# Performance work log

Hardware: AMD Instinct MI355X
Metric: run time of the kernel (lower is better)

Reference implementation:

```python
import jax, jax.numpy as jnp
import numpy as np
import math

N = 100000
E = 1600000
D = 256          # input_size
H = 64           # head_size = input_size // n_heads = 256 // 4


def setup_inputs() -> dict:
    key = jax.random.key(0)
    k1, k2, k3, k4, k5 = jax.random.split(key, 5)
    X = jax.random.normal(k1, (N, D), dtype=jnp.float32)
    edge_index = jax.random.randint(k2, (2, E), 0, N, dtype=jnp.int64)
    # Linear(input_size, head_size, bias=False) weights, stored as [D, H] so Q = X @ Wq
    s = 1.0 / math.sqrt(D)
    Wq = jax.random.uniform(k3, (D, H), dtype=jnp.float32, minval=-s, maxval=s)
    Wk = jax.random.uniform(k4, (D, H), dtype=jnp.float32, minval=-s, maxval=s)
    Wv = jax.random.uniform(k5, (D, H), dtype=jnp.float32, minval=-s, maxval=s)
    return {"X": X, "Wq": Wq, "Wk": Wk, "Wv": Wv, "edge_index": edge_index}


def reference(X, Wq, Wk, Wv, edge_index):
    dk = math.sqrt(H)
    Q = X @ Wq  # [N, H]
    K = X @ Wk
    V = X @ Wv
    src = edge_index[0]  # row of sparse matrix -> softmax segment (dim=1 softmax)
    dst = edge_index[1]  # column -> neighbor supplying K/V
    scores = jnp.sum(Q[src] * K[dst], axis=-1) / dk  # [E]
    # per-row (per src node) stable softmax over edges
    m = jax.ops.segment_max(scores, src, num_segments=N)          # [N], -inf for empty rows
    m = jnp.where(jnp.isfinite(m), m, 0.0)
    e = jnp.exp(scores - m[src])                                   # [E]
    denom = jax.ops.segment_sum(e, src, num_segments=N)            # [N]
    alpha = e / jnp.maximum(denom[src], 1e-38)                     # [E]
    # scatter-weighted V aggregation: out[i] = sum_{(i,j) in edges} alpha_ij * V[j]
    out = jax.ops.segment_sum(alpha[:, None] * V[dst], src, num_segments=N)  # [N, H]
    return out
```

## Files before the change

### kernel.cpp

```cpp
#include <hip/hip_runtime.h>

typedef unsigned short u16;
typedef unsigned int u32;
typedef short short8 __attribute__((ext_vector_type(8)));
typedef float f32x4 __attribute__((ext_vector_type(4)));
typedef u32 u32x4 __attribute__((ext_vector_type(4)));

__device__ __forceinline__ u16 f2bf(float f) {
    union { float f; u32 i; } c; c.f = f;
    u32 i = c.i;
    return (u16)((i + 0x7FFFu + ((i >> 16) & 1u)) >> 16);
}
__device__ __forceinline__ float bf2f(u16 u) {
    union { u32 i; float f; } c; c.i = ((u32)u) << 16; return c.f;
}
__device__ __forceinline__ void bf2x(u32 p, float& lo, float& hi) {
    union { u32 i; float f; } a, b;
    a.i = p << 16; b.i = p & 0xFFFF0000u;
    lo = a.f; hi = b.f;
}
__device__ __forceinline__ u32 cvtpk_bf16(float lo, float hi) {
    u32 r;
    asm("v_cvt_pk_bf16_f32 %0, %1, %2" : "=v"(r) : "v"(lo), "v"(hi));
    return r;
}

__global__ void wfrag_kernel(const float* __restrict__ Wq,
                             const float* __restrict__ Wk,
                             const float* __restrict__ Wv,
                             u16* __restrict__ wf)
{
    int idx = blockIdx.x * 256 + threadIdx.x;
    if (idx >= 12 * 8 * 64) return;
    int lane = idx & 63;
    int s = (idx >> 6) & 7;
    int t = idx >> 9;
    int n = t * 16 + (lane & 15);
    const float* Wsrc = (n < 64) ? Wq : ((n < 128) ? Wk : Wv);
    int col = n & 63;
    int kbase = s * 32 + (lane >> 4) * 8;
    u16 o[8];
#pragma unroll
    for (int j = 0; j < 8; ++j) o[j] = f2bf(Wsrc[(size_t)(kbase + j) * 64 + col]);
    *(short8*)(wf + (size_t)idx * 8) = *(const short8*)o;
}

__global__ __launch_bounds__(256, 2) void qkv_mfma(
    const float* __restrict__ X, const u16* __restrict__ wf,
    float* __restrict__ Qs, u16* __restrict__ Ksb, u16* __restrict__ Vsb,
    int N, int NT)
{
    const int lane = threadIdx.x & 63;
    const int wave = threadIdx.x >> 6;
    const int m    = lane & 15;
    const int quad = lane >> 4;
    const int t0   = wave * 3;

    const short8* wfp = (const short8*)wf;
    short8 bf0[8], bf1[8], bf2[8];
#pragma unroll
    for (int s = 0; s < 8; ++s) {
        bf0[s] = wfp[(size_t)((t0 + 0) * 8 + s) * 64 + lane];
        bf1[s] = wfp[(size_t)((t0 + 1) * 8 + s) * 64 + lane];
        bf2[s] = wfp[(size_t)((t0 + 2) * 8 + s) * 64 + lane];
    }

    for (int tile = blockIdx.x; tile < NT; tile += gridDim.x) {
        int arow = tile * 16 + m;
        if (arow >= N) arow = N - 1;
        const float* xr = X + (size_t)arow * 256 + quad * 8;

        f32x4 acc0 = (f32x4)0.f, acc1 = (f32x4)0.f, acc2 = (f32x4)0.f;

#pragma unroll
        for (int s = 0; s < 8; ++s) {
            float4 a0 = *(const float4*)(xr + s * 32);
            float4 a1 = *(const float4*)(xr + s * 32 + 4);
            union { u32x4 u; short8 s8; } af;
            af.u.x = cvtpk_bf16(a0.x, a0.y);
            af.u.y = cvtpk_bf16(a0.z, a0.w);
            af.u.z = cvtpk_bf16(a1.x, a1.y);
            af.u.w = cvtpk_bf16(a1.z, a1.w);
            acc0 = __builtin_amdgcn_mfma_f32_16x16x32_bf16(af.s8, bf0[s], acc0, 0, 0, 0);
            acc1 = __builtin_amdgcn_mfma_f32_16x16x32_bf16(af.s8, bf1[s], acc1, 0, 0, 0);
            acc2 = __builtin_amdgcn_mfma_f32_16x16x32_bf16(af.s8, bf2[s], acc2, 0, 0, 0);
        }

        int rbase = tile * 16 + quad * 4;
#pragma unroll
        for (int tt = 0; tt < 3; ++tt) {
            int t = t0 + tt;
            f32x4 a = (tt == 0) ? acc0 : ((tt == 1) ? acc1 : acc2);
            int col = (t & 3) * 16 + m;
#pragma unroll
            for (int r = 0; r < 4; ++r) {
                int rr = rbase + r;
                if (rr >= N) continue;
                if (t < 4)      Qs [(size_t)rr * 64 + col] = a[r];
                else if (t < 8) Ksb[(size_t)rr * 64 + col] = f2bf(a[r]);
                else            Vsb[(size_t)rr * 64 + col] = f2bf(a[r]);
            }
        }
    }
}


__global__ __launch_bounds__(256) void count_kernel(
    const int* __restrict__ src, int* __restrict__ bsize,
    int E, int N, int NB, int chunk)
{
    __shared__ int cnt[512];
    for (int i = threadIdx.x; i < 512; i += 256) cnt[i] = 0;
    __syncthreads();
    int lo = blockIdx.x * chunk;
    int hi = min(E, lo + chunk);
    for (int e = lo + (int)threadIdx.x; e < hi; e += 256) {
        int s = src[e];
        if ((unsigned)s < (unsigned)N) atomicAdd(&cnt[s >> 8], 1);
    }
    __syncthreads();
    for (int b = threadIdx.x; b < NB; b += 256)
        if (cnt[b]) atomicAdd(&bsize[b], cnt[b]);
}

__global__ __launch_bounds__(512) void scan391_kernel(
    const int* __restrict__ bsize, int* __restrict__ bbase,
    int* __restrict__ cursor, int* __restrict__ row_ptr_N, int NB)
{
    __shared__ int sd[512];
    int t = threadIdx.x;
    int v = (t < NB) ? bsize[t] : 0;
    sd[t] = v;
    __syncthreads();
    for (int off = 1; off < 512; off <<= 1) {
        int x = (t >= off) ? sd[t - off] : 0;
        __syncthreads();
        sd[t] += x;
        __syncthreads();
    }
    if (t < NB) {
        int excl = sd[t] - v;
        bbase[t] = excl;
        cursor[t] = excl;
        if (t == NB - 1) {
            bbase[NB] = sd[t];
            *row_ptr_N = sd[t];
        }
    }
}

__global__ __launch_bounds__(256) void scatter_pairs_kernel(
    const int* __restrict__ src, const int* __restrict__ dst,
    int* __restrict__ cursor, int2* __restrict__ pairs,
    int E, int N, int NB, int chunk)
{
    __shared__ int cnt[512];
    __shared__ int basei[512];
    for (int i = threadIdx.x; i < 512; i += 256) cnt[i] = 0;
    __syncthreads();
    int lo = blockIdx.x * chunk;
    int hi = min(E, lo + chunk);
    for (int e = lo + (int)threadIdx.x; e < hi; e += 256) {
        int s = src[e];
        if ((unsigned)s < (unsigned)N) atomicAdd(&cnt[s >> 8], 1);
    }
    __syncthreads();
    for (int b = threadIdx.x; b < NB; b += 256)
        basei[b] = cnt[b] ? atomicAdd(&cursor[b], cnt[b]) : 0;
    __syncthreads();
    for (int i = threadIdx.x; i < 512; i += 256) cnt[i] = 0;
    __syncthreads();
    for (int e = lo + (int)threadIdx.x; e < hi; e += 256) {
        int s = src[e];
        if ((unsigned)s >= (unsigned)N) continue;
        int d = dst[e];
        if ((unsigned)d >= (unsigned)N) d = 0;
        int bk = s >> 8;
        int p = basei[bk] + atomicAdd(&cnt[bk], 1);
        pairs[p] = make_int2(s, d);
    }
}

#define MAXB 6144
__global__ __launch_bounds__(256) void sort_bucket_kernel(
    const int2* __restrict__ pairs, const int* __restrict__ bbase,
    int* __restrict__ row_ptr, int* __restrict__ sorted_dst, int N)
{
    __shared__ int deg[256];
    __shared__ int off[256];
    __shared__ int cur[256];
    __shared__ int ldst[MAXB];

    int bk = blockIdx.x;
    int n0 = bk * 256;
    int nn = min(256, N - n0);
    int base = bbase[bk];
    int size = bbase[bk + 1] - base;
    int t = threadIdx.x;

    deg[t] = 0;
    __syncthreads();
    for (int i = t; i < size; i += 256)
        atomicAdd(&deg[pairs[base + i].x & 255], 1);
    __syncthreads();
    off[t] = deg[t];
    __syncthreads();
    for (int s = 1; s < 256; s <<= 1) {
        int x = (t >= s) ? off[t - s] : 0;
        __syncthreads();
        off[t] += x;
        __syncthreads();
    }
    int excl = off[t] - deg[t];
    cur[t] = excl;
    if (t < nn) row_ptr[n0 + t] = base + excl;
    __syncthreads();
    int cap = min(size, MAXB);
    for (int i = t; i < size; i += 256) {
        int2 pr = pairs[base + i];
        int p = atomicAdd(&cur[pr.x & 255], 1);
        if (p < MAXB) ldst[p] = pr.y;
    }
    __syncthreads();
    for (int i = t; i < cap; i += 256)
        sorted_dst[base + i] = ldst[i];
    for (int i = cap + t; i < size; i += 256)
        sorted_dst[base + i] = 0;
}

__global__ __launch_bounds__(256) void attn_csr(
    const float* __restrict__ Qs, const u16* __restrict__ Ksb,
    const u16* __restrict__ Vsb, const int* __restrict__ row_ptr,
    const int* __restrict__ sdst, float* __restrict__ out, int N)
{
    int wid = (int)((blockIdx.x * 256 + threadIdx.x) >> 6);
    if (wid >= N) return;
    int lane = threadIdx.x & 63;
    int sub = lane >> 3;
    int sl  = lane & 7;

    const float* qp = Qs + (size_t)wid * 64 + sl * 8;
    float4 q0 = *(const float4*)(qp);
    float4 q1 = *(const float4*)(qp + 4);

    int beg = row_ptr[wid];
    int end = row_ptr[wid + 1];

    float l = 0.f;
    float a0 = 0.f, a1 = 0.f, a2 = 0.f, a3 = 0.f;
    float a4 = 0.f, a5 = 0.f, a6 = 0.f, a7 = 0.f;

    for (int j = beg; j < end; j += 8) {
        int e = j + sub;
        bool valid = (e < end);
        int d = sdst[valid ? e : beg];

        uint4 kr = *(const uint4*)(Ksb + (size_t)d * 64 + sl * 8);
        float k0, k1, k2, k3, k4, k5, k6, k7;
        bf2x(kr.x, k0, k1); bf2x(kr.y, k2, k3);
        bf2x(kr.z, k4, k5); bf2x(kr.w, k6, k7);

        float p = q0.x * k0 + q0.y * k1 + q0.z * k2 + q0.w * k3
                + q1.x * k4 + q1.y * k5 + q1.z * k6 + q1.w * k7;
        p += __shfl_xor(p, 1);
        p += __shfl_xor(p, 2);
        p += __shfl_xor(p, 4);

        float pe = __expf(p * 0.125f);

        uint4 vr = *(const uint4*)(Vsb + (size_t)d * 64 + sl * 8);
        float v0, v1, v2, v3, v4, v5, v6, v7;
        bf2x(vr.x, v0, v1); bf2x(vr.y, v2, v3);
        bf2x(vr.z, v4, v5); bf2x(vr.w, v6, v7);

        if (valid) {
            l += pe;
            a0 += pe * v0; a1 += pe * v1; a2 += pe * v2; a3 += pe * v3;
            a4 += pe * v4; a5 += pe * v5; a6 += pe * v6; a7 += pe * v7;
        }
    }

#pragma unroll
    for (int off = 8; off <= 32; off <<= 1) {
        l  += __shfl_xor(l, off);
        a0 += __shfl_xor(a0, off); a1 += __shfl_xor(a1, off);
        a2 += __shfl_xor(a2, off); a3 += __shfl_xor(a3, off);
        a4 += __shfl_xor(a4, off); a5 += __shfl_xor(a5, off);
        a6 += __shfl_xor(a6, off); a7 += __shfl_xor(a7, off);
    }

    if (sub == 0) {
        float inv = (l > 0.f) ? (1.f / l) : 0.f;
        float* op = out + (size_t)wid * 64 + sl * 8;
        *(float4*)(op)     = make_float4(a0 * inv, a1 * inv, a2 * inv, a3 * inv);
        *(float4*)(op + 4) = make_float4(a4 * inv, a5 * inv, a6 * inv, a7 * inv);
    }
}

extern "C" void kernel_launch(void* const* d_in, const int* in_sizes, int n_in,
                              void* d_out, int out_size, void* d_ws, size_t ws_size,
                              hipStream_t stream)
{
    const float* X  = (const float*)d_in[0];
    const float* Wq = (const float*)d_in[1];
    const float* Wk = (const float*)d_in[2];
    const float* Wv = (const float*)d_in[3];
    const int*   ei = (const int*)d_in[4];

    const int N = in_sizes[0] / 256;
    const int E = in_sizes[4] / 2;
    const int* src = ei;
    const int* dst = ei + E;
    const int NB = (N + 255) >> 8;

    char* w = (char*)d_ws;
    float* Qs = (float*)w;      w += (size_t)N * 64 * sizeof(float);
    u16* Ksb = (u16*)w;         w += (size_t)N * 64 * sizeof(u16);
    u16* Vsb = (u16*)w;         w += (size_t)N * 64 * sizeof(u16);
    int2* pairs = (int2*)w;     w += (size_t)E * sizeof(int2);
    int* sorted_dst = (int*)w;  w += (size_t)E * sizeof(int);
    int* row_ptr = (int*)w;     w += (size_t)(N + 1) * sizeof(int);
    int* bsize = (int*)w;       w += (size_t)(NB + 1) * sizeof(int);
    int* bbase = (int*)w;       w += (size_t)(NB + 1) * sizeof(int);
    int* cursor = (int*)w;      w += (size_t)(NB + 1) * sizeof(int);
    u16* wf = (u16*)w;          w += (size_t)12 * 8 * 64 * 8 * sizeof(u16);

    hipMemsetAsync(bsize, 0, (size_t)(NB + 1) * sizeof(int), stream);

    const int B1 = 160;
    const int chunk = (E + B1 - 1) / B1;
    const int NT = (N + 15) / 16;

    wfrag_kernel<<<24, 256, 0, stream>>>(Wq, Wk, Wv, wf);
    qkv_mfma<<<768, 256, 0, stream>>>(X, wf, Qs, Ksb, Vsb, N, NT);

    count_kernel<<<B1, 256, 0, stream>>>(src, bsize, E, N, NB, chunk);
    scan391_kernel<<<1, 512, 0, stream>>>(bsize, bbase, cursor, row_ptr + N, NB);
    scatter_pairs_kernel<<<B1, 256, 0, stream>>>(src, dst, cursor, pairs, E, N, NB, chunk);
    sort_bucket_kernel<<<NB, 256, 0, stream>>>(pairs, bbase, row_ptr, sorted_dst, N);

    attn_csr<<<(N * 64 + 255) / 256, 256, 0, stream>>>(
        Qs, Ksb, Vsb, row_ptr, sorted_dst, (float*)d_out, N);
}
```

Before: 358.2 us.

## Stage X tiles in swizzled LDS via direct global-to-LDS loads in QKV GEMM

The QKV projection kernel now loads a 32-row tile of X into shared memory using global_load_lds with an XOR swizzle. All four waves then read their A fragments from LDS, where before each wave re-read X from global memory. Each wave handles two 16-row blocks per tile, so every weight fragment held in registers is reused twice as often. This reduces redundant global traffic for X, at the cost of 32KB of LDS per block, two barriers per tile and more accumulator registers.

```diff
diff --git a/kernel.cpp b/kernel.cpp
--- a/kernel.cpp
+++ b/kernel.cpp
@@ -45,62 +45,93 @@
     *(short8*)(wf + (size_t)idx * 8) = *(const short8*)o;
 }
 
+#define TM 32
 __global__ __launch_bounds__(256, 2) void qkv_mfma(
     const float* __restrict__ X, const u16* __restrict__ wf,
     float* __restrict__ Qs, u16* __restrict__ Ksb, u16* __restrict__ Vsb,
     int N, int NT)
 {
-    const int lane = threadIdx.x & 63;
-    const int wave = threadIdx.x >> 6;
+    __shared__ float xs[TM * 256];
+
+    const int tid  = threadIdx.x;
+    const int lane = tid & 63;
+    const int wave = tid >> 6;
     const int m    = lane & 15;
     const int quad = lane >> 4;
     const int t0   = wave * 3;
 
     const short8* wfp = (const short8*)wf;
-    short8 bf0[8], bf1[8], bf2[8];
+    short8 bfr0[8], bfr1[8], bfr2[8];
 #pragma unroll
     for (int s = 0; s < 8; ++s) {
-        bf0[s] = wfp[(size_t)((t0 + 0) * 8 + s) * 64 + lane];
-        bf1[s] = wfp[(size_t)((t0 + 1) * 8 + s) * 64 + lane];
-        bf2[s] = wfp[(size_t)((t0 + 2) * 8 + s) * 64 + lane];
+        bfr0[s] = wfp[(size_t)((t0 + 0) * 8 + s) * 64 + lane];
+        bfr1[s] = wfp[(size_t)((t0 + 1) * 8 + s) * 64 + lane];
+        bfr2[s] = wfp[(size_t)((t0 + 2) * 8 + s) * 64 + lane];
     }
 
     for (int tile = blockIdx.x; tile < NT; tile += gridDim.x) {
-        int arow = tile * 16 + m;
-        if (arow >= N) arow = N - 1;
-        const float* xr = X + (size_t)arow * 256 + quad * 8;
-
-        f32x4 acc0 = (f32x4)0.f, acc1 = (f32x4)0.f, acc2 = (f32x4)0.f;
-
-#pragma unroll
-        for (int s = 0; s < 8; ++s) {
-            float4 a0 = *(const float4*)(xr + s * 32);
-            float4 a1 = *(const float4*)(xr + s * 32 + 4);
-            union { u32x4 u; short8 s8; } af;
-            af.u.x = cvtpk_bf16(a0.x, a0.y);
-            af.u.y = cvtpk_bf16(a0.z, a0.w);
-            af.u.z = cvtpk_bf16(a1.x, a1.y);
-            af.u.w = cvtpk_bf16(a1.z, a1.w);
-            acc0 = __builtin_amdgcn_mfma_f32_16x16x32_bf16(af.s8, bf0[s], acc0, 0, 0, 0);
-            acc1 = __builtin_amdgcn_mfma_f32_16x16x32_bf16(af.s8, bf1[s], acc1, 0, 0, 0);
-            acc2 = __builtin_amdgcn_mfma_f32_16x16x32_bf16(af.s8, bf2[s], acc2, 0, 0, 0);
-        }
-
-        int rbase = tile * 16 + quad * 4;
-#pragma unroll
-        for (int tt = 0; tt < 3; ++tt) {
-            int t = t0 + tt;
-            f32x4 a = (tt == 0) ? acc0 : ((tt == 1) ? acc1 : acc2);
-            int col = (t & 3) * 16 + m;
-#pragma unroll
-            for (int r = 0; r < 4; ++r) {
-                int rr = rbase + r;
-                if (rr >= N) continue;
-                if (t < 4)      Qs [(size_t)rr * 64 + col] = a[r];
-                else if (t < 8) Ksb[(size_t)rr * 64 + col] = f2bf(a[r]);
-                else            Vsb[(size_t)rr * 64 + col] = f2bf(a[r]);
+#pragma unroll
+        for (int it = 0; it < 8; ++it) {
+            int c0  = (it * 4 + wave) * 64;
+            int c   = c0 + lane;
+            int row = c >> 6;
+            int sblk = (c & 63) ^ (row & 7);
+            int arow = tile * TM + row;
+            if (arow >= N) arow = N - 1;
+            const float* g = X + (size_t)arow * 256 + sblk * 4;
+            float* l = xs + c0 * 4;
+            __builtin_amdgcn_global_load_lds(
+                (const __attribute__((address_space(1))) void*)g,
+                (__attribute__((address_space(3))) void*)l, 16, 0, 0);
+        }
+        __syncthreads();
+
+        f32x4 acc[2][3];
+#pragma unroll
+        for (int rb = 0; rb < 2; ++rb)
+#pragma unroll
+            for (int tt = 0; tt < 3; ++tt) acc[rb][tt] = (f32x4)0.f;
+
+#pragma unroll
+        for (int rb = 0; rb < 2; ++rb) {
+            const int row = rb * 16 + m;
+            const float* xrow = xs + row * 256;
+            const int sw = m & 7;
+#pragma unroll
+            for (int s = 0; s < 8; ++s) {
+                int B0 = quad * 2 + s * 8;
+                float4 a0 = *(const float4*)(xrow + ((B0)     ^ sw) * 4);
+                float4 a1 = *(const float4*)(xrow + ((B0 + 1) ^ sw) * 4);
+                union { u32x4 u; short8 s8; } af;
+                af.u.x = cvtpk_bf16(a0.x, a0.y);
+                af.u.y = cvtpk_bf16(a0.z, a0.w);
+                af.u.z = cvtpk_bf16(a1.x, a1.y);
+                af.u.w = cvtpk_bf16(a1.z, a1.w);
+                acc[rb][0] = __builtin_amdgcn_mfma_f32_16x16x32_bf16(af.s8, bfr0[s], acc[rb][0], 0, 0, 0);
+                acc[rb][1] = __builtin_amdgcn_mfma_f32_16x16x32_bf16(af.s8, bfr1[s], acc[rb][1], 0, 0, 0);
+                acc[rb][2] = __builtin_amdgcn_mfma_f32_16x16x32_bf16(af.s8, bfr2[s], acc[rb][2], 0, 0, 0);
             }
         }
+
+#pragma unroll
+        for (int rb = 0; rb < 2; ++rb) {
+            int rbase = tile * TM + rb * 16 + quad * 4;
+#pragma unroll
+            for (int tt = 0; tt < 3; ++tt) {
+                int t = t0 + tt;
+                int col = (t & 3) * 16 + m;
+#pragma unroll
+                for (int r = 0; r < 4; ++r) {
+                    int rr = rbase + r;
+                    if (rr >= N) continue;
+                    float v = acc[rb][tt][r];
+                    if (t < 4)      Qs [(size_t)rr * 64 + col] = v;
+                    else if (t < 8) Ksb[(size_t)rr * 64 + col] = f2bf(v);
+                    else            Vsb[(size_t)rr * 64 + col] = f2bf(v);
+                }
+            }
+        }
+        __syncthreads();
     }
 }
 
@@ -329,7 +360,7 @@
 
     const int B1 = 160;
     const int chunk = (E + B1 - 1) / B1;
-    const int NT = (N + 15) / 16;
+    const int NT = (N + TM - 1) / TM;
 
     wfrag_kernel<<<24, 256, 0, stream>>>(Wq, Wk, Wv, wf);
     qkv_mfma<<<768, 256, 0, stream>>>(X, wf, Qs, Ksb, Vsb, N, NT);
```

Result: faster. 339.1 us (-5.3%).
